# Kernel tuning notes

Measured on AMD Instinct MI355X. Metric: run time of the kernel, lower is better.

Reference implementation:

```python
import jax, jax.numpy as jnp
import numpy as np

M = 2          # n_mix
D_K = 128      # feature dim
TEMP = float(np.sqrt(D_K))  # temperature = d_k ** 0.5


def setup_inputs() -> dict:
    key = jax.random.key(0)
    k1, k2, k3, k4 = jax.random.split(key, 4)
    BS, N, N2 = 8, 2048, 2048
    qt = jax.random.normal(k1, (BS, N, D_K), jnp.float32)
    kt = jax.random.normal(k2, (BS, N2, D_K), jnp.float32)
    vt = jax.random.normal(k3, (BS, N2, D_K), jnp.float32)
    std = M ** -0.5
    kernel = jax.random.uniform(k4, (M, D_K), jnp.float32, -std, std)
    return {"qt": qt, "kt": kt, "vt": vt, "kernel": kernel}


def reference(qt, kt, vt, kernel):
    # channels_last path of MixtureOfSoftMaxACF.call, training=False (dropout = identity)
    BS, N, dk = qt.shape
    N2 = kt.shape[1]
    d = dk // M
    # mixture prior: softmax(kernel @ mean_q^T) over axis=1 (faithful to Softmax(axis=1))
    bar_qt = jnp.mean(qt, axis=1)                       # (BS, dk)
    prior_mix = jax.nn.softmax(kernel @ bar_qt.T, axis=1)  # (m, BS)
    prior_mix = prior_mix.reshape(BS * M, 1, 1)            # row-major reshape, as in TF
    # split features into mixtures via row-major reshape (as tf.reshape does)
    q = qt.reshape(BS * M, N, d)
    k = kt.reshape(BS * M, N2, d)
    att = jnp.einsum('bnd,bmd->bnm', q, k) / TEMP        # (BS*m, N, N2)
    att = jax.nn.softmax(att, axis=2)
    att = (att * prior_mix).reshape(BS, M, N, N2).sum(axis=1)  # (BS, N, N2)
    return att @ vt                                      # (BS, N, d_v)
```

## Files before the change

kernel.cpp:

```cpp
#include <hip/hip_runtime.h>
#include <hip/hip_fp16.h>

typedef float    f32x4 __attribute__((ext_vector_type(4)));
typedef _Float16 f16x2 __attribute__((ext_vector_type(2)));
typedef _Float16 f16x4 __attribute__((ext_vector_type(4)));
typedef _Float16 f16x8 __attribute__((ext_vector_type(8)));

#define BS 8
#define NN 2048
#define DK 128
#define DM 64
#define MIXOFF (1024 * DK)
#define QSCALE 0.12751744116926208f

#define MFMA32(a, b, c) __builtin_amdgcn_mfma_f32_16x16x32_f16((a), (b), (c), 0, 0, 0)
#define EXP2(x) __builtin_amdgcn_exp2f(x)

__device__ __forceinline__ f16x2 pkrtz(float x, float y) {
  return __builtin_bit_cast(f16x2, __builtin_amdgcn_cvt_pkrtz(x, y));
}

__device__ __forceinline__ void load_lds16(const _Float16* g, _Float16* l) {
  __builtin_amdgcn_global_load_lds(
      (const __attribute__((address_space(1))) void*)(uintptr_t)g,
      (__attribute__((address_space(3))) void*)(uint32_t)(uintptr_t)l, 16, 0, 0);
}

__global__ void prep_k(const float* __restrict__ kt, _Float16* __restrict__ kh,
                       const float* __restrict__ vt, _Float16* __restrict__ vT,
                       const float* __restrict__ qt, float* __restrict__ partial) {
  __shared__ float tile[64][65];
  __shared__ float red[256];
  int blk = blockIdx.x;
  int t = threadIdx.x;
  if (blk < 512) {
    size_t base = (size_t)blk * 4096;
#pragma unroll
    for (int j = 0; j < 4; ++j) {
      size_t i = base + j * 1024 + t * 4;
      f32x4 v = *(const f32x4*)(kt + i);
      f16x4 h;
      h[0] = (_Float16)v[0]; h[1] = (_Float16)v[1];
      h[2] = (_Float16)v[2]; h[3] = (_Float16)v[3];
      *(f16x4*)(kh + i) = h;
    }
  } else if (blk < 1024) {
    int i2 = blk - 512;
    int b = i2 >> 6;
    int rem = i2 & 63;
    int j0 = (rem & 31) * 64;
    int c0 = (rem >> 5) * 64;
    int tx = t & 63, ty = t >> 6;
    const float* src = vt + ((size_t)b * NN + j0) * DK + c0;
#pragma unroll
    for (int rr = 0; rr < 16; ++rr) {
      int row = ty * 16 + rr;
      tile[row][tx] = src[(size_t)row * DK + tx];
    }
    __syncthreads();
    _Float16* dst = vT + ((size_t)b * DK + c0) * NN + j0;
    int chl = t >> 4;
    int k4 = (t & 15) * 4;
#pragma unroll
    for (int r2 = 0; r2 < 4; ++r2) {
      int ch = r2 * 16 + chl;
      f16x4 h;
      h[0] = (_Float16)tile[k4 + 0][ch]; h[1] = (_Float16)tile[k4 + 1][ch];
      h[2] = (_Float16)tile[k4 + 2][ch]; h[3] = (_Float16)tile[k4 + 3][ch];
      *(f16x4*)(dst + (size_t)ch * NN + k4) = h;
    }
  } else {
    int i = blk - 1024;
    int b = i >> 3, seg = i & 7;
    int c = t & 127, h = t >> 7;
    const float* p = qt + ((size_t)b * NN + seg * 256 + h * 128) * DK + c;
    float s = 0.f;
#pragma unroll 8
    for (int n = 0; n < 128; ++n) s += p[(size_t)n * DK];
    red[t] = s;
    __syncthreads();
    if (t < 128) partial[(size_t)i * 128 + t] = red[t] + red[t + 128];
  }
}

#define STAGE(BUF, IT) do {                                                     \
    _Float16* dst0_ = stg + (BUF) * 8192;                                       \
    _Pragma("unroll")                                                           \
    for (int j_ = 0; j_ < 4; ++j_) {                                            \
      int unit_ = j_ * 256 + (int)threadIdx.x;                                  \
      const _Float16* g_;                                                       \
      if (unit_ < 512) {                                                        \
        int mix_ = unit_ >> 8, qq_ = unit_ & 255, r_ = qq_ >> 3;                \
        int uu_ = (qq_ & 7) ^ ((r_ & 3) ^ ((r_ >> 3) << 1));                    \
        g_ = kh + bq + mix_ * MIXOFF + (size_t)((IT) * 32 + r_) * 64 + uu_ * 8; \
      } else {                                                                  \
        int qq_ = unit_ - 512, ch_ = qq_ >> 2;                                  \
        int uu_ = (qq_ & 3) ^ ((ch_ + (ch_ >> 2)) & 3);                         \
        g_ = vT + bV + (size_t)ch_ * NN + (IT) * 32 + uu_ * 8;                  \
      }                                                                         \
      load_lds16(g_, dst0_ + unit_ * 8);                                        \
    }                                                                           \
  } while (0)

#define ITER(BUF, IT) do {                                                      \
    __syncthreads(); \
    if ((IT) + 1 < 64) STAGE((BUF) ^ 1, (IT) + 1);                              \
    const _Float16* sb_ = stg + (BUF) * 8192;                                   \
    f16x8 kf[8], vf[8];                                                         \
    kf[0] = *(const f16x8*)(sb_ + kr0 + kA);                                    \
    kf[1] = *(const f16x8*)(sb_ + kr0 + kB);                                    \
    kf[2] = *(const f16x8*)(sb_ + 2048 + kr0 + kA);                             \
    kf[3] = *(const f16x8*)(sb_ + 2048 + kr0 + kB);                             \
    kf[4] = *(const f16x8*)(sb_ + kr1 + kA);                                    \
    kf[5] = *(const f16x8*)(sb_ + kr1 + kB);                                    \
    kf[6] = *(const f16x8*)(sb_ + 2048 + kr1 + kA);                             \
    kf[7] = *(const f16x8*)(sb_ + 2048 + kr1 + kB);                             \
    _Pragma("unroll")                                                           \
    for (int cc = 0; cc < 8; ++cc)                                              \
      vf[cc] = *(const f16x8*)(sb_ + vbase + cc * 512);                         \
    f32x4 s[2][2];                                                              \
    s[0][0] = MFMA32(kf[1], qf[0][1], MFMA32(kf[0], qf[0][0], z));              \
    s[1][0] = MFMA32(kf[3], qf[1][1], MFMA32(kf[2], qf[1][0], z));              \
    s[0][1] = MFMA32(kf[5], qf[0][1], MFMA32(kf[4], qf[0][0], z));              \
    s[1][1] = MFMA32(kf[7], qf[1][1], MFMA32(kf[6], qf[1][0], z));              \
    _Pragma("unroll")                                                           \
    for (int m = 0; m < 2; ++m) {                                               \
      union { f16x8 v; f16x2 h[4]; } w_;                                        \
      w_.h[0] = pkrtz(EXP2(s[m][0][0]), EXP2(s[m][0][1]));                      \
      w_.h[1] = pkrtz(EXP2(s[m][0][2]), EXP2(s[m][0][3]));                      \
      w_.h[2] = pkrtz(EXP2(s[m][1][0]), EXP2(s[m][1][1]));                      \
      w_.h[3] = pkrtz(EXP2(s[m][1][2]), EXP2(s[m][1][3]));                      \
      lacc[m] = MFMA32(ones, w_.v, lacc[m]);                                    \
      _Pragma("unroll")                                                         \
      for (int cc = 0; cc < 8; ++cc)                                            \
        acc[m][cc] = MFMA32(vf[cc], w_.v, acc[m][cc]);                          \
    }                                                                           \
  } while (0)

__global__ __launch_bounds__(256) void attn_k(const float* __restrict__ qt,
                                              const _Float16* __restrict__ kh,
                                              const _Float16* __restrict__ vT,
                                              const float* __restrict__ kern,
                                              const float* __restrict__ partial,
                                              float* __restrict__ out) {
  __shared__ __align__(16) char smem[40960];
  _Float16* stg = (_Float16*)smem;
  const int b = blockIdx.x & 7;
  const int qb = blockIdx.x >> 3;
  const int wv = threadIdx.x >> 6;
  const int lane = threadIdx.x & 63;
  const int quad = lane >> 4, l16 = lane & 15;
  const int perm = ((l16 >> 2) << 3) | (l16 & 3);
  const size_t bq = (size_t)b * (NN * DK);
  const size_t bV = (size_t)b * (DK * NN);
  const int q0 = qb * 64 + wv * 16;

  f16x8 qf[2][2];
#pragma unroll
  for (int m = 0; m < 2; ++m)
#pragma unroll
    for (int c = 0; c < 2; ++c) {
      const float* qp = qt + bq + (size_t)m * (1024 * DK) +
                        (size_t)(q0 + l16) * DM + quad * 8 + c * 32;
      f32x4 v0 = *(const f32x4*)qp;
      f32x4 v1 = *(const f32x4*)(qp + 4);
      union { f16x8 v; f16x2 h[4]; } w;
      w.h[0] = pkrtz(v0[0] * QSCALE, v0[1] * QSCALE);
      w.h[1] = pkrtz(v0[2] * QSCALE, v0[3] * QSCALE);
      w.h[2] = pkrtz(v1[0] * QSCALE, v1[1] * QSCALE);
      w.h[3] = pkrtz(v1[2] * QSCALE, v1[3] * QSCALE);
      qf[m][c] = w.v;
    }

  const int gK = (l16 & 3) ^ ((l16 >> 2) << 1);
  const int hV = (l16 + (l16 >> 2)) & 3;
  const int kA = (quad ^ gK) * 8;
  const int kB = ((quad + 4) ^ gK) * 8;
  const int kr0 = perm * 64;
  const int kr1 = (perm + 4) * 64;
  const int vbase = 4096 + l16 * 32 + (quad ^ hV) * 8;

  const f32x4 z = {0.f, 0.f, 0.f, 0.f};
  f32x4 acc[2][8];
  f32x4 lacc[2];
#pragma unroll
  for (int m = 0; m < 2; ++m) {
    lacc[m] = z;
#pragma unroll
    for (int cc = 0; cc < 8; ++cc) acc[m][cc] = z;
  }
  const _Float16 one = (_Float16)1.0f;
  const f16x8 ones = {one, one, one, one, one, one, one, one};

  STAGE(0, 0);
  for (int it = 0; it < 64; it += 2) {
    ITER(0, it);
    ITER(1, it + 1);
  }

  __syncthreads();
  float* obuf = (float*)smem;
  float* barL = (float*)(smem + 33792);
  float* lgp = (float*)(smem + 33792 + 4096);
  float* exq = lgp + 16;
  float* prp = lgp + 32;

  for (int e = threadIdx.x; e < 1024; e += 256) {
    int bb = e >> 7, c = e & 127;
    float s = 0.f;
#pragma unroll
    for (int seg = 0; seg < 8; ++seg) s += partial[(size_t)(bb * 8 + seg) * 128 + c];
    barL[bb * 128 + c] = s * (1.0f / 2048.0f);
  }
  __syncthreads();
  if (threadIdx.x < 16) {
    int m = threadIdx.x >> 3, bb = threadIdx.x & 7;
    float s = 0.f;
    for (int c = 0; c < DK; ++c) s += kern[m * DK + c] * barL[bb * 128 + c];
    lgp[threadIdx.x] = s;
  }
  __syncthreads();
  if (threadIdx.x < 16) {
    int m = threadIdx.x >> 3;
    float mx = lgp[m * 8];
    for (int i = 1; i < 8; ++i) mx = fmaxf(mx, lgp[m * 8 + i]);
    exq[threadIdx.x] = __expf(lgp[threadIdx.x] - mx);
  }
  __syncthreads();
  if (threadIdx.x < 16) {
    int m = threadIdx.x >> 3;
    float sm = 0.f;
    for (int i = 0; i < 8; ++i) sm += exq[m * 8 + i];
    prp[threadIdx.x] = exq[threadIdx.x] / sm;
  }
  __syncthreads();
  const float w0 = prp[b * 2 + 0], w1 = prp[b * 2 + 1];
  const float r0 = w0 / lacc[0][0];
  const float r1 = w1 / lacc[1][0];
#pragma unroll
  for (int cc = 0; cc < 8; ++cc) {
    f32x4 o;
#pragma unroll
    for (int e = 0; e < 4; ++e) o[e] = acc[0][cc][e] * r0 + acc[1][cc][e] * r1;
    *(f32x4*)&obuf[(wv * 16 + l16) * 132 + cc * 16 + quad * 4] = o;
  }
  __syncthreads();
  const int row = threadIdx.x >> 2;
  const int w = row >> 4, ql = row & 15;
  const int cb = (threadIdx.x & 3) * 4;
  float* op = out + ((size_t)b * NN + qb * 64 + row) * DK;
#pragma unroll
  for (int g2 = 0; g2 < 8; ++g2)
    *(f32x4*)(op + cb + g2 * 16) = *(const f32x4*)&obuf[(w * 16 + ql) * 132 + cb + g2 * 16];
}

extern "C" void kernel_launch(void* const* d_in, const int* in_sizes, int n_in,
                              void* d_out, int out_size, void* d_ws, size_t ws_size,
                              hipStream_t stream) {
  const float* qt = (const float*)d_in[0];
  const float* kt = (const float*)d_in[1];
  const float* vt = (const float*)d_in[2];
  const float* kern = (const float*)d_in[3];
  float* out = (float*)d_out;

  char* ws = (char*)d_ws;
  float* partial = (float*)ws;
  _Float16* khp = (_Float16*)(ws + 65536);
  _Float16* vTp = khp + (size_t)BS * NN * DK;

  prep_k<<<dim3(1088), dim3(256), 0, stream>>>(kt, khp, vt, vTp, qt, partial);
  attn_k<<<dim3(256), dim3(256), 0, stream>>>(qt, khp, vTp, kern, partial, out);
}
```

Measured before the change: 126.2 us.

## Split KV range across 8 waves per block with in-LDS partial reduction

Each block now runs 512 threads (8 waves). Every wave handles 32 query rows. Waves are split by K-half within a tile and by tile parity, and tiles of 64 keys are staged per step. The row-sum now uses scalar float adds instead of an MFMA against a ones vector. Partial accumulators are merged through LDS atomics before the prior-weighted output is written. This raises work per block and reuse of K/V fragments, in exchange for more registers, a larger LDS footprint (64KB) and an atomic reduction epilogue.

New measurement: 186.2 us. 1.48x slower.

```diff
diff --git a/kernel.cpp b/kernel.cpp
--- a/kernel.cpp
+++ b/kernel.cpp
@@ -83,94 +83,103 @@
   }
 }
 
-#define STAGE(BUF, IT) do {                                                     \
-    _Float16* dst0_ = stg + (BUF) * 8192;                                       \
-    _Pragma("unroll")                                                           \
-    for (int j_ = 0; j_ < 4; ++j_) {                                            \
-      int unit_ = j_ * 256 + (int)threadIdx.x;                                  \
-      const _Float16* g_;                                                       \
-      if (unit_ < 512) {                                                        \
-        int mix_ = unit_ >> 8, qq_ = unit_ & 255, r_ = qq_ >> 3;                \
-        int uu_ = (qq_ & 7) ^ ((r_ & 3) ^ ((r_ >> 3) << 1));                    \
-        g_ = kh + bq + mix_ * MIXOFF + (size_t)((IT) * 32 + r_) * 64 + uu_ * 8; \
-      } else {                                                                  \
-        int qq_ = unit_ - 512, ch_ = qq_ >> 2;                                  \
-        int uu_ = (qq_ & 3) ^ ((ch_ + (ch_ >> 2)) & 3);                         \
-        g_ = vT + bV + (size_t)ch_ * NN + (IT) * 32 + uu_ * 8;                  \
-      }                                                                         \
-      load_lds16(g_, dst0_ + unit_ * 8);                                        \
-    }                                                                           \
+#define STAGE(BUF, S) do {                                                \
+    _Float16* db_ = stg + (BUF) * 16384;                                  \
+    load_lds16(khg + gK0 + (S) * 2048, db_ + t * 8);                      \
+    load_lds16(vTg + gV0 + (S) * 32, db_ + 4096 + t * 8);                 \
+    load_lds16(khg + gK1 + (S) * 2048, db_ + 8192 + t * 8);               \
+    load_lds16(vTg + gV1 + (S) * 32, db_ + 12288 + t * 8);                \
   } while (0)
 
-#define ITER(BUF, IT) do {                                                      \
-    __syncthreads(); \
-    if ((IT) + 1 < 64) STAGE((BUF) ^ 1, (IT) + 1);                              \
-    const _Float16* sb_ = stg + (BUF) * 8192;                                   \
-    f16x8 kf[8], vf[8];                                                         \
-    kf[0] = *(const f16x8*)(sb_ + kr0 + kA);                                    \
-    kf[1] = *(const f16x8*)(sb_ + kr0 + kB);                                    \
-    kf[2] = *(const f16x8*)(sb_ + 2048 + kr0 + kA);                             \
-    kf[3] = *(const f16x8*)(sb_ + 2048 + kr0 + kB);                             \
-    kf[4] = *(const f16x8*)(sb_ + kr1 + kA);                                    \
-    kf[5] = *(const f16x8*)(sb_ + kr1 + kB);                                    \
-    kf[6] = *(const f16x8*)(sb_ + 2048 + kr1 + kA);                             \
-    kf[7] = *(const f16x8*)(sb_ + 2048 + kr1 + kB);                             \
-    _Pragma("unroll")                                                           \
-    for (int cc = 0; cc < 8; ++cc)                                              \
-      vf[cc] = *(const f16x8*)(sb_ + vbase + cc * 512);                         \
-    f32x4 s[2][2];                                                              \
-    s[0][0] = MFMA32(kf[1], qf[0][1], MFMA32(kf[0], qf[0][0], z));              \
-    s[1][0] = MFMA32(kf[3], qf[1][1], MFMA32(kf[2], qf[1][0], z));              \
-    s[0][1] = MFMA32(kf[5], qf[0][1], MFMA32(kf[4], qf[0][0], z));              \
-    s[1][1] = MFMA32(kf[7], qf[1][1], MFMA32(kf[6], qf[1][0], z));              \
-    _Pragma("unroll")                                                           \
-    for (int m = 0; m < 2; ++m) {                                               \
-      union { f16x8 v; f16x2 h[4]; } w_;                                        \
-      w_.h[0] = pkrtz(EXP2(s[m][0][0]), EXP2(s[m][0][1]));                      \
-      w_.h[1] = pkrtz(EXP2(s[m][0][2]), EXP2(s[m][0][3]));                      \
-      w_.h[2] = pkrtz(EXP2(s[m][1][0]), EXP2(s[m][1][1]));                      \
-      w_.h[3] = pkrtz(EXP2(s[m][1][2]), EXP2(s[m][1][3]));                      \
-      lacc[m] = MFMA32(ones, w_.v, lacc[m]);                                    \
-      _Pragma("unroll")                                                         \
-      for (int cc = 0; cc < 8; ++cc)                                            \
-        acc[m][cc] = MFMA32(vf[cc], w_.v, acc[m][cc]);                          \
-    }                                                                           \
+#define COMPUTE(BUF) do {                                                      \
+    const _Float16* sb_ = stg + (BUF) * 16384 + khs * 8192;                    \
+    f16x8 kf_[8];                                                              \
+    kf_[0] = *(const f16x8*)(sb_ + kr0 + kA);                                  \
+    kf_[1] = *(const f16x8*)(sb_ + kr0 + kB);                                  \
+    kf_[2] = *(const f16x8*)(sb_ + 2048 + kr0 + kA);                           \
+    kf_[3] = *(const f16x8*)(sb_ + 2048 + kr0 + kB);                           \
+    kf_[4] = *(const f16x8*)(sb_ + kr1 + kA);                                  \
+    kf_[5] = *(const f16x8*)(sb_ + kr1 + kB);                                  \
+    kf_[6] = *(const f16x8*)(sb_ + 2048 + kr1 + kA);                           \
+    kf_[7] = *(const f16x8*)(sb_ + 2048 + kr1 + kB);                           \
+    f32x4 s_[2][2][2];                                    \
+    _Pragma("unroll")                                                          \
+    for (int u = 0; u < 2; ++u) {                                              \
+      s_[u][0][0] = MFMA32(kf_[1], qf[u][0][1], MFMA32(kf_[0], qf[u][0][0], z)); \
+      s_[u][1][0] = MFMA32(kf_[3], qf[u][1][1], MFMA32(kf_[2], qf[u][1][0], z)); \
+      s_[u][0][1] = MFMA32(kf_[5], qf[u][0][1], MFMA32(kf_[4], qf[u][0][0], z)); \
+      s_[u][1][1] = MFMA32(kf_[7], qf[u][1][1], MFMA32(kf_[6], qf[u][1][0], z)); \
+    }                                                                          \
+    f16x8 vf_[8];                                                              \
+    _Pragma("unroll")                                                          \
+    for (int cc = 0; cc < 8; ++cc)                                             \
+      vf_[cc] = *(const f16x8*)(sb_ + vbase + cc * 512);                       \
+    _Pragma("unroll")                                                          \
+    for (int u = 0; u < 2; ++u)                                                \
+      _Pragma("unroll")                                                        \
+      for (int m = 0; m < 2; ++m) {                                            \
+        float e0 = EXP2(s_[u][m][0][0]), e1 = EXP2(s_[u][m][0][1]);            \
+        float e2 = EXP2(s_[u][m][0][2]), e3 = EXP2(s_[u][m][0][3]);            \
+        float e4 = EXP2(s_[u][m][1][0]), e5 = EXP2(s_[u][m][1][1]);            \
+        float e6 = EXP2(s_[u][m][1][2]), e7 = EXP2(s_[u][m][1][3]);            \
+        lsum[u][m] += ((e0 + e1) + (e2 + e3)) + ((e4 + e5) + (e6 + e7));       \
+        union { f16x8 v; f16x2 h[4]; } w_;                                     \
+        w_.h[0] = pkrtz(e0, e1); w_.h[1] = pkrtz(e2, e3);                      \
+        w_.h[2] = pkrtz(e4, e5); w_.h[3] = pkrtz(e6, e7);                      \
+        _Pragma("unroll")                                                      \
+        for (int cc = 0; cc < 8; ++cc)                                         \
+          acc[u][m][cc] = MFMA32(vf_[cc], w_.v, acc[u][m][cc]);                \
+      }                                                                        \
   } while (0)
 
-__global__ __launch_bounds__(256) void attn_k(const float* __restrict__ qt,
-                                              const _Float16* __restrict__ kh,
-                                              const _Float16* __restrict__ vT,
-                                              const float* __restrict__ kern,
-                                              const float* __restrict__ partial,
-                                              float* __restrict__ out) {
-  __shared__ __align__(16) char smem[40960];
+__global__ __launch_bounds__(512, 2) void attn_k(const float* __restrict__ qt,
+                                                 const _Float16* __restrict__ khg,
+                                                 const _Float16* __restrict__ vTg,
+                                                 const float* __restrict__ kern,
+                                                 const float* __restrict__ partial,
+                                                 float* __restrict__ out) {
+  __shared__ __align__(16) char smem[65536];
   _Float16* stg = (_Float16*)smem;
   const int b = blockIdx.x & 7;
   const int qb = blockIdx.x >> 3;
-  const int wv = threadIdx.x >> 6;
-  const int lane = threadIdx.x & 63;
+  const int t = threadIdx.x;
+  const int wv = t >> 6;
+  const int qp = wv & 1, khs = (wv >> 1) & 1, par = wv >> 2;
+  const int lane = t & 63;
   const int quad = lane >> 4, l16 = lane & 15;
   const int perm = ((l16 >> 2) << 3) | (l16 & 3);
-  const size_t bq = (size_t)b * (NN * DK);
-  const size_t bV = (size_t)b * (DK * NN);
-  const int q0 = qb * 64 + wv * 16;
-
-  f16x8 qf[2][2];
-#pragma unroll
-  for (int m = 0; m < 2; ++m)
-#pragma unroll
-    for (int c = 0; c < 2; ++c) {
-      const float* qp = qt + bq + (size_t)m * (1024 * DK) +
-                        (size_t)(q0 + l16) * DM + quad * 8 + c * 32;
-      f32x4 v0 = *(const f32x4*)qp;
-      f32x4 v1 = *(const f32x4*)(qp + 4);
-      union { f16x8 v; f16x2 h[4]; } w;
-      w.h[0] = pkrtz(v0[0] * QSCALE, v0[1] * QSCALE);
-      w.h[1] = pkrtz(v0[2] * QSCALE, v0[3] * QSCALE);
-      w.h[2] = pkrtz(v1[0] * QSCALE, v1[1] * QSCALE);
-      w.h[3] = pkrtz(v1[2] * QSCALE, v1[3] * QSCALE);
-      qf[m][c] = w.v;
-    }
+  const int bq = b * (NN * DK);
+  const int bV = b * (DK * NN);
+
+  f16x8 qf[2][2][2];
+#pragma unroll
+  for (int u = 0; u < 2; ++u)
+#pragma unroll
+    for (int m = 0; m < 2; ++m)
+#pragma unroll
+      for (int c = 0; c < 2; ++c) {
+        const float* qp_ = qt + bq + m * MIXOFF +
+                           (qb * 64 + qp * 32 + u * 16 + l16) * DM + quad * 8 + c * 32;
+        f32x4 v0 = *(const f32x4*)qp_;
+        f32x4 v1 = *(const f32x4*)(qp_ + 4);
+        union { f16x8 v; f16x2 h[4]; } w;
+        w.h[0] = pkrtz(v0[0] * QSCALE, v0[1] * QSCALE);
+        w.h[1] = pkrtz(v0[2] * QSCALE, v0[3] * QSCALE);
+        w.h[2] = pkrtz(v1[0] * QSCALE, v1[1] * QSCALE);
+        w.h[3] = pkrtz(v1[2] * QSCALE, v1[3] * QSCALE);
+        qf[u][m][c] = w.v;
+      }
+
+  const int mixu = (t >> 8) & 1;
+  const int w8 = t & 255;
+  const int rK = w8 >> 3;
+  const int uuK = (w8 & 7) ^ ((rK & 3) ^ ((rK >> 3) << 1));
+  const int chV = t >> 2;
+  const int uuV = (t & 3) ^ ((chV + (chV >> 2)) & 3);
+  const int gK0 = bq + mixu * MIXOFF + rK * 64 + uuK * 8;
+  const int gK1 = gK0 + 1024 * 64;
+  const int gV0 = bV + chV * NN + uuV * 8;
+  const int gV1 = gV0 + 1024;
 
   const int gK = (l16 & 3) ^ ((l16 >> 2) << 1);
   const int hV = (l16 + (l16 >> 2)) & 3;
@@ -181,77 +190,116 @@
   const int vbase = 4096 + l16 * 32 + (quad ^ hV) * 8;
 
   const f32x4 z = {0.f, 0.f, 0.f, 0.f};
-  f32x4 acc[2][8];
-  f32x4 lacc[2];
-#pragma unroll
-  for (int m = 0; m < 2; ++m) {
-    lacc[m] = z;
-#pragma unroll
-    for (int cc = 0; cc < 8; ++cc) acc[m][cc] = z;
-  }
-  const _Float16 one = (_Float16)1.0f;
-  const f16x8 ones = {one, one, one, one, one, one, one, one};
+  f32x4 acc[2][2][8];
+  float lsum[2][2] = {{0.f, 0.f}, {0.f, 0.f}};
+#pragma unroll
+  for (int u = 0; u < 2; ++u)
+#pragma unroll
+    for (int m = 0; m < 2; ++m)
+#pragma unroll
+      for (int cc = 0; cc < 8; ++cc) acc[u][m][cc] = z;
 
   STAGE(0, 0);
-  for (int it = 0; it < 64; it += 2) {
-    ITER(0, it);
-    ITER(1, it + 1);
-  }
-
-  __syncthreads();
+  for (int s = 0; s < 32; s += 2) {
+    __syncthreads();
+    STAGE(1, s + 1);
+    if (par == 0) COMPUTE(0);
+    __syncthreads();
+    if (s + 2 < 32) STAGE(0, s + 2);
+    if (par == 1) COMPUTE(1);
+  }
+  __syncthreads();
+
   float* obuf = (float*)smem;
   float* barL = (float*)(smem + 33792);
-  float* lgp = (float*)(smem + 33792 + 4096);
-  float* exq = lgp + 16;
-  float* prp = lgp + 32;
-
-  for (int e = threadIdx.x; e < 1024; e += 256) {
+  float* lgp = (float*)(smem + 37888);
+  float* exq = (float*)(smem + 37952);
+  float* prp = (float*)(smem + 38016);
+
+  for (int e = t; e < 1024; e += 512) {
     int bb = e >> 7, c = e & 127;
-    float s = 0.f;
-#pragma unroll
-    for (int seg = 0; seg < 8; ++seg) s += partial[(size_t)(bb * 8 + seg) * 128 + c];
-    barL[bb * 128 + c] = s * (1.0f / 2048.0f);
-  }
-  __syncthreads();
-  if (threadIdx.x < 16) {
-    int m = threadIdx.x >> 3, bb = threadIdx.x & 7;
-    float s = 0.f;
-    for (int c = 0; c < DK; ++c) s += kern[m * DK + c] * barL[bb * 128 + c];
-    lgp[threadIdx.x] = s;
-  }
-  __syncthreads();
-  if (threadIdx.x < 16) {
-    int m = threadIdx.x >> 3;
+    float ss = 0.f;
+#pragma unroll
+    for (int seg = 0; seg < 8; ++seg) ss += partial[(size_t)(bb * 8 + seg) * 128 + c];
+    barL[e] = ss * (1.0f / 2048.0f);
+  }
+  __syncthreads();
+  if (t < 16) {
+    int m = t >> 3, bb = t & 7;
+    float ss = 0.f;
+    for (int c = 0; c < DK; ++c) ss += kern[m * DK + c] * barL[bb * 128 + c];
+    lgp[t] = ss;
+  }
+  __syncthreads();
+  if (t < 16) {
+    int m = t >> 3;
     float mx = lgp[m * 8];
     for (int i = 1; i < 8; ++i) mx = fmaxf(mx, lgp[m * 8 + i]);
-    exq[threadIdx.x] = __expf(lgp[threadIdx.x] - mx);
-  }
-  __syncthreads();
-  if (threadIdx.x < 16) {
-    int m = threadIdx.x >> 3;
+    exq[t] = __expf(lgp[t] - mx);
+  }
+  __syncthreads();
+  if (t < 16) {
+    int m = t >> 3;
     float sm = 0.f;
     for (int i = 0; i < 8; ++i) sm += exq[m * 8 + i];
-    prp[threadIdx.x] = exq[threadIdx.x] / sm;
+    prp[t] = exq[t] / sm;
   }
   __syncthreads();
   const float w0 = prp[b * 2 + 0], w1 = prp[b * 2 + 1];
-  const float r0 = w0 / lacc[0][0];
-  const float r1 = w1 / lacc[1][0];
-#pragma unroll
-  for (int cc = 0; cc < 8; ++cc) {
-    f32x4 o;
-#pragma unroll
-    for (int e = 0; e < 4; ++e) o[e] = acc[0][cc][e] * r0 + acc[1][cc][e] * r1;
-    *(f32x4*)&obuf[(wv * 16 + l16) * 132 + cc * 16 + quad * 4] = o;
-  }
-  __syncthreads();
-  const int row = threadIdx.x >> 2;
-  const int w = row >> 4, ql = row & 15;
-  const int cb = (threadIdx.x & 3) * 4;
-  float* op = out + ((size_t)b * NN + qb * 64 + row) * DK;
-#pragma unroll
-  for (int g2 = 0; g2 < 8; ++g2)
-    *(f32x4*)(op + cb + g2 * 16) = *(const f32x4*)&obuf[(w * 16 + ql) * 132 + cb + g2 * 16];
+  const int row = t >> 3;
+  const int cb = (t & 7) * 16;
+  f32x4 o0[4];
+
+#pragma unroll
+  for (int M = 0; M < 2; ++M) {
+    if (t < 64) obuf[t * 132 + 128] = 0.f;
+    if (wv < 2) {
+#pragma unroll
+      for (int u = 0; u < 2; ++u) {
+        int r_ = (qp * 32 + u * 16 + l16) * 132;
+#pragma unroll
+        for (int cc = 0; cc < 8; ++cc)
+          *(f32x4*)&obuf[r_ + cc * 16 + quad * 4] = acc[u][M][cc];
+      }
+    }
+    __syncthreads();
+    if (wv >= 2) {
+#pragma unroll
+      for (int u = 0; u < 2; ++u) {
+        int r_ = (qp * 32 + u * 16 + l16) * 132;
+#pragma unroll
+        for (int cc = 0; cc < 8; ++cc)
+#pragma unroll
+          for (int e = 0; e < 4; ++e)
+            atomicAdd(&obuf[r_ + cc * 16 + quad * 4 + e], acc[u][M][cc][e]);
+      }
+    }
+#pragma unroll
+    for (int u = 0; u < 2; ++u)
+      atomicAdd(&obuf[(qp * 32 + u * 16 + l16) * 132 + 128], lsum[u][M]);
+    __syncthreads();
+    if (M == 0) {
+      float r0 = w0 / obuf[row * 132 + 128];
+#pragma unroll
+      for (int g = 0; g < 4; ++g) {
+        f32x4 v = *(const f32x4*)&obuf[row * 132 + cb + g * 4];
+#pragma unroll
+        for (int e = 0; e < 4; ++e) o0[g][e] = v[e] * r0;
+      }
+      __syncthreads();
+    } else {
+      float r1 = w1 / obuf[row * 132 + 128];
+      float* op = out + ((size_t)b * NN + qb * 64 + row) * DK + cb;
+#pragma unroll
+      for (int g = 0; g < 4; ++g) {
+        f32x4 v = *(const f32x4*)&obuf[row * 132 + cb + g * 4];
+        f32x4 o;
+#pragma unroll
+        for (int e = 0; e < 4; ++e) o[e] = o0[g][e] + v[e] * r1;
+        *(f32x4*)(op + g * 4) = o;
+      }
+    }
+  }
 }
 
 extern "C" void kernel_launch(void* const* d_in, const int* in_sizes, int n_in,
@@ -269,5 +317,5 @@
   _Float16* vTp = khp + (size_t)BS * NN * DK;
 
   prep_k<<<dim3(1088), dim3(256), 0, stream>>>(kt, khp, vt, vTp, qt, partial);
-  attn_k<<<dim3(256), dim3(256), 0, stream>>>(qt, khp, vTp, kern, partial, out);
-}
+  attn_k<<<dim3(256), dim3(512), 0, stream>>>(qt, khp, vTp, kern, partial, out);
+}
```
